# Optimization experiments

Measured on AMD Instinct MI355X. Metric: run time of the kernel, lower is better.

## Reference

```python
import jax, jax.numpy as jnp
import numpy as np

# Config: B=16, channels C=16, feature_num D=4, node_num K=128, L=128, emb E=10
# c_in for the 1x1 conv = (order*support_len + 1) * C = (2*3 + 1)*16 = 112

def setup_inputs() -> dict:
    key = jax.random.key(0)
    ks = jax.random.split(key, 8)
    B, C, D, K, L, E = 16, 16, 4, 128, 128, 10
    return {
        "x": jax.random.normal(ks[0], (B, C, D * K * L), dtype=jnp.float32),
        "supports": jax.random.uniform(ks[1], (2, K, K), dtype=jnp.float32),
        "nodevec1": jax.random.normal(ks[2], (D, K, E), dtype=jnp.float32),
        "nodevec2": jax.random.normal(ks[3], (D, E, K), dtype=jnp.float32),
        "imp_W": jax.random.normal(ks[4], (K, K), dtype=jnp.float32) * 0.05,
        "imp_b": jax.random.normal(ks[5], (K,), dtype=jnp.float32) * 0.05,
        "mlp_W": jax.random.normal(ks[6], (D, C, 7 * C), dtype=jnp.float32) * 0.05,
        "mlp_b": jax.random.normal(ks[7], (D, C), dtype=jnp.float32) * 0.05,
        "B": B, "C": C, "D": D, "K": K, "L": L,
    }


def reference(x, supports, nodevec1, nodevec2, imp_W, imp_b, mlp_W, mlp_b, B, C, D, K, L):
    # x: (B, C, D*K*L) -> (D, B*L, C, K)  [matches reshape/permute in torch forward]
    xr = x.reshape(B, C, D, K, L).transpose(2, 0, 4, 1, 3).reshape(D, B * L, C, K)

    # adaptive adjacency per feature
    # torch: importance = Linear(nv1.T).T  => imp[j,e] = sum_k W[j,k] nv1[k,e] + b[j]
    imp = jnp.einsum('jk,fke->fje', imp_W, nodevec1) + imp_b[None, :, None]
    nv1m = nodevec1 * imp                                   # (D, K, E)
    scores = jnp.einsum('fke,fej->fkj', nv1m, nodevec2)     # (D, K, K)
    adp = jax.nn.softmax(jax.nn.relu(scores), axis=2)       # softmax over dim=1 of (K,K)

    # multi-hop diffusion: out[n,c,w] = sum_v x[n,c,v] * a[w,v], order=2
    outs = [xr]
    for s in range(2):  # two shared supports
        a = supports[s]
        x1 = jnp.einsum('fncv,wv->fncw', xr, a)
        x2 = jnp.einsum('fncv,wv->fncw', x1, a)
        outs.append(x1)
        outs.append(x2)
    x1 = jnp.einsum('fncv,fwv->fncw', xr, adp)  # per-feature adaptive support
    x2 = jnp.einsum('fncv,fwv->fncw', x1, adp)
    outs.append(x1)
    outs.append(x2)

    cat = jnp.concatenate(outs, axis=2)  # (D, B*L, 7C, K)

    # per-feature 1x1 conv = channel GEMM
    y = jnp.einsum('fnck,foc->fnok', cat, mlp_W) + mlp_b[:, None, :, None]  # (D, N, C, K)

    y = y.reshape(D, B, L, C, K)
    y = jnp.transpose(y, (1, 2, 0, 3, 4))  # (B, L, D, C, K) == torch.stack(res, dim=2)
    y = jnp.transpose(y, (0, 3, 2, 4, 1))  # (B, C, D, K, L)
    return y.reshape(B, C, D * K * L)
```

## Files before the change

### kernel.cpp

```cpp
#include <hip/hip_runtime.h>
#include <hip/hip_bf16.h>


namespace {

constexpr int Kn = 128;
constexpr int En = 10;

typedef __attribute__((ext_vector_type(8))) short short8;
typedef __attribute__((ext_vector_type(4))) float f32x4;

__device__ inline unsigned short f2bf(float f) {
    unsigned x = __float_as_uint(f);
    return (unsigned short)((x + 0x7FFFu + ((x >> 16) & 1u)) >> 16);
}
__device__ inline unsigned pack2(float lo, float hi) {
    return (unsigned)f2bf(lo) | ((unsigned)f2bf(hi) << 16);
}
__device__ inline unsigned pack2b(float lo, float hi) {
    union { __hip_bfloat162 h; unsigned u; } cv;
    float2 f; f.x = lo; f.y = hi;
    cv.h = __float22bfloat162_rn(f);
    return cv.u;
}

__global__ __launch_bounds__(256) void build_adj(
    const float* __restrict__ supports,
    const float* __restrict__ nv1,
    const float* __restrict__ nv2,
    const float* __restrict__ impW,
    const float* __restrict__ impB,
    float* __restrict__ mats)
{
    const int tid = threadIdx.x;
    const int blk = blockIdx.x;
    if (blk < 2) {
        const float* A = supports + blk * Kn * Kn;
        float* dst = mats + (blk * 2) * Kn * Kn;
        for (int i = tid; i < Kn * Kn; i += 256) dst[i] = A[i];
        return;
    }
    const int d = blk - 2;
    __shared__ float nv1m[Kn * En];
    __shared__ float nv2s[En * Kn];
    for (int i = tid; i < Kn * En; i += 256) nv1m[i] = nv1[d * Kn * En + i];
    for (int i = tid; i < En * Kn; i += 256) nv2s[i] = nv2[d * En * Kn + i];
    __syncthreads();
    float impv[5];
    #pragma unroll
    for (int r = 0; r < 5; ++r) {
        const int idx = tid + r * 256;
        const int j = idx / En, e = idx - j * En;
        float acc = impB[j];
        for (int kk = 0; kk < Kn; ++kk)
            acc += impW[j * Kn + kk] * nv1m[kk * En + e];
        impv[r] = acc;
    }
    __syncthreads();
    #pragma unroll
    for (int r = 0; r < 5; ++r) nv1m[tid + r * 256] *= impv[r];
    __syncthreads();
    if (tid < Kn) {
        const int k = tid;
        float a[En];
        #pragma unroll
        for (int e = 0; e < En; ++e) a[e] = nv1m[k * En + e];
        float mx = 0.f;
        for (int j = 0; j < Kn; ++j) {
            float s = 0.f;
            #pragma unroll
            for (int e = 0; e < En; ++e) s += a[e] * nv2s[e * Kn + j];
            mx = fmaxf(mx, s);
        }
        float sum = 0.f;
        for (int j = 0; j < Kn; ++j) {
            float s = 0.f;
            #pragma unroll
            for (int e = 0; e < En; ++e) s += a[e] * nv2s[e * Kn + j];
            s = fmaxf(s, 0.f);
            sum += expf(s - mx);
        }
        const float inv = 1.f / sum;
        float* dst = mats + (4 + d) * Kn * Kn;
        for (int j = 0; j < Kn; ++j) {
            float s = 0.f;
            #pragma unroll
            for (int e = 0; e < En; ++e) s += a[e] * nv2s[e * Kn + j];
            s = fmaxf(s, 0.f);
            dst[k * Kn + j] = expf(s - mx) * inv;
        }
    }
}

__global__ __launch_bounds__(256) void square_cvt(
    const float* __restrict__ fm, unsigned short* __restrict__ wbm)
{
    const int tid = threadIdx.x;
    if (blockIdx.x < 96) {
        __shared__ float S[Kn * Kn];
        const int m = blockIdx.x >> 4, strip = blockIdx.x & 15;
        const int src = (m == 0) ? 0 : (m == 1) ? 2 : (2 + m);
        const int dst = (m == 0) ? 2 : (m == 1) ? 4 : (2 + 2 * m);
        const float* s = fm + src * Kn * Kn;
        unsigned short* o = wbm + dst * Kn * Kn;
        for (int i = tid; i < Kn * Kn; i += 256) S[i] = s[i];
        __syncthreads();
        const int v = strip * 8 + (tid >> 5);
        const int k0 = (tid & 31) * 4;
        float acc0 = 0.f, acc1 = 0.f, acc2 = 0.f, acc3 = 0.f;
        for (int u0 = 0; u0 < Kn; u0 += 4) {
            const float4 av = *reinterpret_cast<const float4*>(&S[v * Kn + u0]);
            const float a[4] = {av.x, av.y, av.z, av.w};
            #pragma unroll
            for (int j = 0; j < 4; ++j) {
                const float4 m4 = *reinterpret_cast<const float4*>(&S[(u0 + j) * Kn + k0]);
                acc0 += a[j] * m4.x; acc1 += a[j] * m4.y;
                acc2 += a[j] * m4.z; acc3 += a[j] * m4.w;
            }
        }
        uint2 r;
        r.x = pack2(acc0, acc1);
        r.y = pack2(acc2, acc3);
        *reinterpret_cast<uint2*>(&o[v * Kn + k0]) = r;
    } else {
        const int s = blockIdx.x - 96;
        const int wslot = (s == 0) ? 0 : (s == 1) ? 1 : (s == 2) ? 3 : (5 + 2 * (s - 3));
        const int fsrc  = (s == 0) ? -1 : (s == 1) ? 0 : (s == 2) ? 2 : (4 + (s - 3));
        for (int i = tid; i < Kn * Kn; i += 256) {
            const int k = i >> 7, v = i & 127;
            const float val = (fsrc < 0) ? ((k == v) ? 1.f : 0.f) : fm[fsrc * 16384 + i];
            wbm[wslot * 16384 + i] = f2bf(val);
        }
    }
}

__global__ __launch_bounds__(256, 3) void fused_mfma(
    const float* __restrict__ x,
    const unsigned short* __restrict__ wbm,
    const float* __restrict__ mlpW,
    const float* __restrict__ mlpB,
    float* __restrict__ out)
{
    __shared__ __align__(16) char lds[49216];
    const int tid = threadIdx.x;
    const int lane = tid & 63, lr = lane & 15, lg = lane >> 4;
    const int wid = tid >> 6, wr = wid >> 1, wk = wid & 1;

    const unsigned u = blockIdx.x;
    const unsigned pid = (u & 7) * 256 + (u >> 3);
    const int kh = pid & 1;
    const int lt = (pid >> 1) & 15;
    const int b  = (pid >> 5) & 15;
    const int d  = (int)(pid >> 9);
    const int l0 = lt * 8;

    const f32x4 zero4 = {0.f, 0.f, 0.f, 0.f};
    short8 Mb[8];
    const unsigned short* mbase = wbm + kh * 8192 + wk * 4096 + lr * 128 + lg * 8;

    auto loadM = [&](int slot) {
        const unsigned short* mp = mbase + slot * 16384;
        #pragma unroll
        for (int j = 0; j < 2; ++j)
            #pragma unroll
            for (int ks = 0; ks < 4; ++ks)
                Mb[j * 4 + ks] =
                    *reinterpret_cast<const short8*>(mp + j * 2048 + ks * 32);
    };

    loadM(0);

    {
        const int half = tid & 1;
        const int p5 = (tid >> 1) & 31;
        #pragma unroll
        for (int i = 0; i < 8; ++i) {
            const int g = i * 4 + wid;
            const int c = g >> 1, pg = g & 1;
            const int p = pg * 32 + p5;
            const int v = p * 2;
            const float* p0 = x + (size_t)b * 1048576 + c * 65536 + d * 16384 +
                              v * 128 + l0 + half * 4;
            const float4 q0 = *reinterpret_cast<const float4*>(p0);
            const float4 q1 = *reinterpret_cast<const float4*>(p0 + 128);
            const float a0[4] = {q0.x, q0.y, q0.z, q0.w};
            const float a1[4] = {q1.x, q1.y, q1.z, q1.w};
            const int colb = (4 * p) ^ ((c & 7) << 4);
            #pragma unroll
            for (int j = 0; j < 4; ++j) {
                const int n = half * 4 + j;
                *reinterpret_cast<unsigned*>(lds + (n * 16 + c) * 256 + colb) =
                    pack2b(a0[j], a1[j]);
            }
        }
    }
    if (tid < 8) *reinterpret_cast<unsigned*>(lds + 49152 + tid * 4) = 0u;

    short8 Wf[4];
    #pragma unroll
    for (int p = 0; p < 4; ++p) {
        short8 w;
        #pragma unroll
        for (int j = 0; j < 8; ++j) {
            const int tc = lg * 8 + j, t = 2 * p + (tc >> 4), c = tc & 15;
            const float wv = (t < 7) ? mlpW[d * 1792 + lr * 112 + t * 16 + c] : 0.f;
            w[j] = (short)f2bf(wv);
        }
        Wf[p] = w;
    }

    __syncthreads();

    const int xrow = wr * 16384 + lr * 256;
    const int xcol = (lg * 16) ^ ((lr & 7) << 4);
    char* zb = lds + 32768;

    f32x4 Y[4][2];
    #pragma unroll
    for (int ni = 0; ni < 4; ++ni) {
        Y[ni][0] = zero4; Y[ni][1] = zero4;
    }

    auto phaseA_Z = [&]() {
        f32x4 D[4][2];
        #pragma unroll
        for (int rti = 0; rti < 4; ++rti) { D[rti][0] = zero4; D[rti][1] = zero4; }
        #pragma unroll
        for (int ks = 0; ks < 4; ++ks) {
            const char* xaddr = lds + xrow + (xcol ^ (ks * 64));
            #pragma unroll
            for (int rti = 0; rti < 4; ++rti) {
                const short8 Xk = *reinterpret_cast<const short8*>(xaddr + rti * 4096);
                D[rti][0] = __builtin_amdgcn_mfma_f32_16x16x32_bf16(
                    Xk, Mb[ks], D[rti][0], 0, 0, 0);
                D[rti][1] = __builtin_amdgcn_mfma_f32_16x16x32_bf16(
                    Xk, Mb[4 + ks], D[rti][1], 0, 0, 0);
            }
        }
        #pragma unroll
        for (int rti = 0; rti < 4; ++rti) {
            #pragma unroll
            for (int j = 0; j < 2; ++j) {
                const int n = wr * 4 + rti;
                const int kp = (wk * 2 + j) * 16 + lr;
                uint2 zz;
                zz.x = pack2b(D[rti][j][0], D[rti][j][1]);
                zz.y = pack2b(D[rti][j][2], D[rti][j][3]);
                *reinterpret_cast<uint2*>(zb + n * 2048 + kp * 32 + lg * 8) = zz;
            }
        }
    };

    auto phaseB = [&](int p, int parity) {
        short8 Wm;
        const bool keep_lo = (parity == 0);
        #pragma unroll
        for (int j = 0; j < 8; ++j)
            Wm[j] = ((lg < 2) == keep_lo) ? Wf[p][j] : (short)0;
        const bool data_lane = ((lg < 2) == keep_lo);
        #pragma unroll
        for (int ni = 0; ni < 4; ++ni) {
            const int n = wr * 4 + ni;
            #pragma unroll
            for (int ktl = 0; ktl < 2; ++ktl) {
                const int kp = wk * 32 + ktl * 16 + lr;
                const char* zp = data_lane
                    ? (zb + n * 2048 + kp * 32 + (lg & 1) * 16)
                    : (lds + 49152 + (lg & 1) * 16);
                const short8 Bfz = *reinterpret_cast<const short8*>(zp);
                Y[ni][ktl] = __builtin_amdgcn_mfma_f32_16x16x32_bf16(
                    Wm, Bfz, Y[ni][ktl], 0, 0, 0);
            }
        }
    };

    phaseA_Z();  loadM(1);          phaseB(0, 0);
    phaseA_Z();  loadM(2);          phaseB(0, 1);
    phaseA_Z();  loadM(3);          phaseB(1, 0);
    phaseA_Z();  loadM(4);          phaseB(1, 1);
    phaseA_Z();  loadM(5 + 2 * d);  phaseB(2, 0);
    phaseA_Z();  loadM(6 + 2 * d);  phaseB(2, 1);
    phaseA_Z();                     phaseB(3, 0);

    __syncthreads();

    #pragma unroll
    for (int ni = 0; ni < 4; ++ni) {
        const int l = wr * 4 + ni;
        #pragma unroll
        for (int ktl = 0; ktl < 2; ++ktl) {
            const int k = wk * 32 + ktl * 16 + lr;
            #pragma unroll
            for (int r = 0; r < 4; ++r) {
                const int o = lg * 4 + r;
                *reinterpret_cast<float*>(
                    lds + o * 2048 + k * 32 + ((l * 4) ^ (k & 12))) = Y[ni][ktl][r];
            }
        }
    }
    __syncthreads();

    {
        const int half = tid & 1;
        const int klo = (tid >> 1) & 31;
        #pragma unroll
        for (int i = 0; i < 8; ++i) {
            const int g = i * 4 + wid;
            const int o = g >> 1, kg = g & 1;
            const int k = kg * 32 + klo;
            const int pp = (k >> 2) & 3;
            const float4 F = *reinterpret_cast<const float4*>(
                lds + o * 2048 + k * 32 + half * 16);
            float4 s1, s2;
            if (pp & 1) { s1.x = F.y; s1.y = F.x; s1.z = F.w; s1.w = F.z; }
            else        { s1 = F; }
            if (pp & 2) { s2.x = s1.z; s2.y = s1.w; s2.z = s1.x; s2.w = s1.y; }
            else        { s2 = s1; }
            const float bv = mlpB[d * 16 + o];
            s2.x += bv; s2.y += bv; s2.z += bv; s2.w += bv;
            float* gp = out + (size_t)b * 1048576 + o * 65536 + d * 16384 +
                        (kh * 64 + k) * 128 + l0 + half * 4;
            *reinterpret_cast<float4*>(gp) = s2;
        }
    }
}

}

extern "C" void kernel_launch(void* const* d_in, const int* in_sizes, int n_in,
                              void* d_out, int out_size, void* d_ws, size_t ws_size,
                              hipStream_t stream)
{
    const float* x    = (const float*)d_in[0];
    const float* sup  = (const float*)d_in[1];
    const float* nv1  = (const float*)d_in[2];
    const float* nv2  = (const float*)d_in[3];
    const float* impW = (const float*)d_in[4];
    const float* impB = (const float*)d_in[5];
    const float* mlpW = (const float*)d_in[6];
    const float* mlpB = (const float*)d_in[7];
    float* outp = (float*)d_out;

    float* fm = (float*)d_ws;
    unsigned short* wbm = (unsigned short*)((char*)d_ws + 786432);

    build_adj<<<6, 256, 0, stream>>>(sup, nv1, nv2, impW, impB, fm);
    square_cvt<<<103, 256, 0, stream>>>(fm, wbm);
    fused_mfma<<<2048, 256, 0, stream>>>(x, wbm, mlpW, mlpB, outp);
}
```

Baseline: 139.3 us.

## Interleave per-tile diffusion and channel MFMA with per-wave Z scratch for occupancy

Fuses the two phases so each row tile's diffusion result is packed to a small per-wave LDS scratch and immediately consumed by the channel-mixing MFMA. This drops the shared Z buffer and zero-pad region, shrinking LDS from about 48KB to 40KB, and raises launch bounds to 4 blocks per CU. Keeping only one tile of intermediate accumulators live also lowers register pressure. The risk is that masked lanes now read real Z data instead of a zero pad, so correctness relies on the zeroed weight lanes, and the next-M load is moved inside the loop.

```diff
diff --git a/kernel.cpp b/kernel.cpp
--- a/kernel.cpp
+++ b/kernel.cpp
@@ -134,14 +134,14 @@
     }
 }
 
-__global__ __launch_bounds__(256, 3) void fused_mfma(
+__global__ __launch_bounds__(256, 4) void fused_mfma(
     const float* __restrict__ x,
     const unsigned short* __restrict__ wbm,
     const float* __restrict__ mlpW,
     const float* __restrict__ mlpB,
     float* __restrict__ out)
 {
-    __shared__ __align__(16) char lds[49216];
+    __shared__ __align__(16) char lds[40960];
     const int tid = threadIdx.x;
     const int lane = tid & 63, lr = lane & 15, lg = lane >> 4;
     const int wid = tid >> 6, wr = wid >> 1, wk = wid & 1;
@@ -194,7 +194,6 @@
             }
         }
     }
-    if (tid < 8) *reinterpret_cast<unsigned*>(lds + 49152 + tid * 4) = 0u;
 
     short8 Wf[4];
     #pragma unroll
@@ -213,74 +212,52 @@
 
     const int xrow = wr * 16384 + lr * 256;
     const int xcol = (lg * 16) ^ ((lr & 7) << 4);
-    char* zb = lds + 32768;
+    char* zb = lds + 32768 + wid * 2048;
 
     f32x4 Y[4][2];
     #pragma unroll
-    for (int ni = 0; ni < 4; ++ni) {
-        Y[ni][0] = zero4; Y[ni][1] = zero4;
-    }
-
-    auto phaseA_Z = [&]() {
-        f32x4 D[4][2];
-        #pragma unroll
-        for (int rti = 0; rti < 4; ++rti) { D[rti][0] = zero4; D[rti][1] = zero4; }
-        #pragma unroll
-        for (int ks = 0; ks < 4; ++ks) {
-            const char* xaddr = lds + xrow + (xcol ^ (ks * 64));
-            #pragma unroll
-            for (int rti = 0; rti < 4; ++rti) {
-                const short8 Xk = *reinterpret_cast<const short8*>(xaddr + rti * 4096);
-                D[rti][0] = __builtin_amdgcn_mfma_f32_16x16x32_bf16(
-                    Xk, Mb[ks], D[rti][0], 0, 0, 0);
-                D[rti][1] = __builtin_amdgcn_mfma_f32_16x16x32_bf16(
-                    Xk, Mb[4 + ks], D[rti][1], 0, 0, 0);
-            }
-        }
-        #pragma unroll
-        for (int rti = 0; rti < 4; ++rti) {
-            #pragma unroll
-            for (int j = 0; j < 2; ++j) {
-                const int n = wr * 4 + rti;
-                const int kp = (wk * 2 + j) * 16 + lr;
-                uint2 zz;
-                zz.x = pack2b(D[rti][j][0], D[rti][j][1]);
-                zz.y = pack2b(D[rti][j][2], D[rti][j][3]);
-                *reinterpret_cast<uint2*>(zb + n * 2048 + kp * 32 + lg * 8) = zz;
-            }
-        }
-    };
-
-    auto phaseB = [&](int p, int parity) {
+    for (int ni = 0; ni < 4; ++ni) { Y[ni][0] = zero4; Y[ni][1] = zero4; }
+
+    auto do_t = [&](int p, int parity, int nextSlot) {
         short8 Wm;
         const bool keep_lo = (parity == 0);
         #pragma unroll
         for (int j = 0; j < 8; ++j)
             Wm[j] = ((lg < 2) == keep_lo) ? Wf[p][j] : (short)0;
-        const bool data_lane = ((lg < 2) == keep_lo);
-        #pragma unroll
-        for (int ni = 0; ni < 4; ++ni) {
-            const int n = wr * 4 + ni;
+        #pragma unroll
+        for (int rti = 0; rti < 4; ++rti) {
+            f32x4 D0 = zero4, D1 = zero4;
+            #pragma unroll
+            for (int ks = 0; ks < 4; ++ks) {
+                const short8 Xk = *reinterpret_cast<const short8*>(
+                    lds + xrow + (xcol ^ (ks * 64)) + rti * 4096);
+                D0 = __builtin_amdgcn_mfma_f32_16x16x32_bf16(Xk, Mb[ks], D0, 0, 0, 0);
+                D1 = __builtin_amdgcn_mfma_f32_16x16x32_bf16(Xk, Mb[4 + ks], D1, 0, 0, 0);
+            }
+            if (rti == 3 && nextSlot >= 0) loadM(nextSlot);
+            char* zs = zb + (rti & 1) * 1024;
+            uint2 z0, z1;
+            z0.x = pack2b(D0[0], D0[1]); z0.y = pack2b(D0[2], D0[3]);
+            z1.x = pack2b(D1[0], D1[1]); z1.y = pack2b(D1[2], D1[3]);
+            *reinterpret_cast<uint2*>(zs + lr * 32 + lg * 8) = z0;
+            *reinterpret_cast<uint2*>(zs + 512 + lr * 32 + lg * 8) = z1;
             #pragma unroll
             for (int ktl = 0; ktl < 2; ++ktl) {
-                const int kp = wk * 32 + ktl * 16 + lr;
-                const char* zp = data_lane
-                    ? (zb + n * 2048 + kp * 32 + (lg & 1) * 16)
-                    : (lds + 49152 + (lg & 1) * 16);
-                const short8 Bfz = *reinterpret_cast<const short8*>(zp);
-                Y[ni][ktl] = __builtin_amdgcn_mfma_f32_16x16x32_bf16(
-                    Wm, Bfz, Y[ni][ktl], 0, 0, 0);
+                const short8 Bfz = *reinterpret_cast<const short8*>(
+                    zs + ktl * 512 + lr * 32 + (lg & 1) * 16);
+                Y[rti][ktl] = __builtin_amdgcn_mfma_f32_16x16x32_bf16(
+                    Wm, Bfz, Y[rti][ktl], 0, 0, 0);
             }
         }
     };
 
-    phaseA_Z();  loadM(1);          phaseB(0, 0);
-    phaseA_Z();  loadM(2);          phaseB(0, 1);
-    phaseA_Z();  loadM(3);          phaseB(1, 0);
-    phaseA_Z();  loadM(4);          phaseB(1, 1);
-    phaseA_Z();  loadM(5 + 2 * d);  phaseB(2, 0);
-    phaseA_Z();  loadM(6 + 2 * d);  phaseB(2, 1);
-    phaseA_Z();                     phaseB(3, 0);
+    do_t(0, 0, 1);
+    do_t(0, 1, 2);
+    do_t(1, 0, 3);
+    do_t(1, 1, 4);
+    do_t(2, 0, 5 + 2 * d);
+    do_t(2, 1, 6 + 2 * d);
+    do_t(3, 0, -1);
 
     __syncthreads();
 
```

New measurement: 149.6 us. 7.3% more time.

## Pad Z staging buffer rows and split adaptive softmax across all threads

Applied to the files above, without the earlier changes.

The Z intermediate buffer in LDS gets a padded row stride (40 bytes per kp row, 2560 per n) to reduce bank conflicts on the packed writes and reads. Because of the padding, the 16-byte reads become two 8-byte loads. Separately, the adjacency softmax kernel now uses all 256 threads, each handling half of a row, with a shared-memory reduction for max and sum. The costs are more LDS per block, which may affect occupancy at 3 blocks per CU, and extra LDS read instructions.

```diff
diff --git a/kernel.cpp b/kernel.cpp
--- a/kernel.cpp
+++ b/kernel.cpp
@@ -43,6 +43,7 @@
     const int d = blk - 2;
     __shared__ float nv1m[Kn * En];
     __shared__ float nv2s[En * Kn];
+    __shared__ float red[256];
     for (int i = tid; i < Kn * En; i += 256) nv1m[i] = nv1[d * Kn * En + i];
     for (int i = tid; i < En * Kn; i += 256) nv2s[i] = nv2[d * En * Kn + i];
     __syncthreads();
@@ -60,34 +61,39 @@
     #pragma unroll
     for (int r = 0; r < 5; ++r) nv1m[tid + r * 256] *= impv[r];
     __syncthreads();
-    if (tid < Kn) {
-        const int k = tid;
+    {
+        const int k = tid & 127, hf = tid >> 7;
+        const int j0 = hf * 64;
         float a[En];
         #pragma unroll
         for (int e = 0; e < En; ++e) a[e] = nv1m[k * En + e];
         float mx = 0.f;
-        for (int j = 0; j < Kn; ++j) {
+        for (int j = j0; j < j0 + 64; ++j) {
             float s = 0.f;
             #pragma unroll
             for (int e = 0; e < En; ++e) s += a[e] * nv2s[e * Kn + j];
             mx = fmaxf(mx, s);
         }
+        red[tid] = mx;
+        __syncthreads();
+        mx = fmaxf(red[tid], red[tid ^ 128]);
+        __syncthreads();
         float sum = 0.f;
-        for (int j = 0; j < Kn; ++j) {
+        for (int j = j0; j < j0 + 64; ++j) {
             float s = 0.f;
             #pragma unroll
             for (int e = 0; e < En; ++e) s += a[e] * nv2s[e * Kn + j];
-            s = fmaxf(s, 0.f);
-            sum += expf(s - mx);
-        }
-        const float inv = 1.f / sum;
+            sum += expf(fmaxf(s, 0.f) - mx);
+        }
+        red[tid] = sum;
+        __syncthreads();
+        const float inv = 1.f / (red[tid] + red[tid ^ 128]);
         float* dst = mats + (4 + d) * Kn * Kn;
-        for (int j = 0; j < Kn; ++j) {
+        for (int j = j0; j < j0 + 64; ++j) {
             float s = 0.f;
             #pragma unroll
             for (int e = 0; e < En; ++e) s += a[e] * nv2s[e * Kn + j];
-            s = fmaxf(s, 0.f);
-            dst[k * Kn + j] = expf(s - mx) * inv;
+            dst[k * Kn + j] = expf(fmaxf(s, 0.f) - mx) * inv;
         }
     }
 }
@@ -141,7 +147,7 @@
     const float* __restrict__ mlpB,
     float* __restrict__ out)
 {
-    __shared__ __align__(16) char lds[49216];
+    __shared__ __align__(16) char lds[53280];
     const int tid = threadIdx.x;
     const int lane = tid & 63, lr = lane & 15, lg = lane >> 4;
     const int wid = tid >> 6, wr = wid >> 1, wk = wid & 1;
@@ -194,7 +200,7 @@
             }
         }
     }
-    if (tid < 8) *reinterpret_cast<unsigned*>(lds + 49152 + tid * 4) = 0u;
+    if (tid < 8) *reinterpret_cast<unsigned*>(lds + 53248 + tid * 4) = 0u;
 
     short8 Wf[4];
     #pragma unroll
@@ -213,13 +219,11 @@
 
     const int xrow = wr * 16384 + lr * 256;
     const int xcol = (lg * 16) ^ ((lr & 7) << 4);
-    char* zb = lds + 32768;
+    char* zbase = lds + 32768;
 
     f32x4 Y[4][2];
     #pragma unroll
-    for (int ni = 0; ni < 4; ++ni) {
-        Y[ni][0] = zero4; Y[ni][1] = zero4;
-    }
+    for (int ni = 0; ni < 4; ++ni) { Y[ni][0] = zero4; Y[ni][1] = zero4; }
 
     auto phaseA_Z = [&]() {
         f32x4 D[4][2];
@@ -246,7 +250,7 @@
                 uint2 zz;
                 zz.x = pack2b(D[rti][j][0], D[rti][j][1]);
                 zz.y = pack2b(D[rti][j][2], D[rti][j][3]);
-                *reinterpret_cast<uint2*>(zb + n * 2048 + kp * 32 + lg * 8) = zz;
+                *reinterpret_cast<uint2*>(zbase + n * 2560 + kp * 40 + lg * 8) = zz;
             }
         }
     };
@@ -265,11 +269,13 @@
             for (int ktl = 0; ktl < 2; ++ktl) {
                 const int kp = wk * 32 + ktl * 16 + lr;
                 const char* zp = data_lane
-                    ? (zb + n * 2048 + kp * 32 + (lg & 1) * 16)
-                    : (lds + 49152 + (lg & 1) * 16);
-                const short8 Bfz = *reinterpret_cast<const short8*>(zp);
+                    ? (zbase + n * 2560 + kp * 40 + (lg & 1) * 16)
+                    : (lds + 53248 + (lg & 1) * 16);
+                union { short8 s; uint2 uu[2]; } bf;
+                bf.uu[0] = *reinterpret_cast<const uint2*>(zp);
+                bf.uu[1] = *reinterpret_cast<const uint2*>(zp + 8);
                 Y[ni][ktl] = __builtin_amdgcn_mfma_f32_16x16x32_bf16(
-                    Wm, Bfz, Y[ni][ktl], 0, 0, 0);
+                    Wm, bf.s, Y[ni][ktl], 0, 0, 0);
             }
         }
     };
```

After: 132.4 us. 5.0% less time.
